# Kernel tuning notes

Measured on AMD Instinct MI355X. Metric: run time of the kernel, lower is better.

## Reference

```python
import jax, jax.numpy as jnp
import numpy as np


def setup_inputs() -> dict:
    key = jax.random.key(0)
    k1, k2 = jax.random.split(key)
    x = jax.random.normal(k1, (8, 128, 192, 192), dtype=jnp.float32)  # [n, c, h, w]
    K = jax.random.normal(k2, (8, 128, 128), dtype=jnp.float32)      # [n, Q, c]
    return {"x": x, "K": K}


def reference(x, K):
    n, c, h, w = x.shape
    xf = x.reshape(n, c, h * w)                      # [n, c, HW]
    # scores: [n, HW, Q] = x^T @ K^T (unscaled)
    y = jnp.einsum("ncs,nqc->nsq", xf, K)
    # softmax over spatial dim (HW), matching torch.softmax(y, dim=1)
    y = jax.nn.softmax(y, axis=1)
    # summary: [n, Q, c] = y^T @ x^T
    summary = jnp.einsum("nsq,ncs->nqc", y, xf)
    return summary
```

## Files before the change

### kernel.cpp

```cpp
#include <hip/hip_runtime.h>
#include <cstdint>


#define HW_DIM 36864
#define L2E 1.44269504088896340736f

typedef _Float16 half8 __attribute__((ext_vector_type(8)));
typedef float f32x16 __attribute__((ext_vector_type(16)));

#if __has_builtin(__builtin_amdgcn_exp2f)
#define EXP2(x) __builtin_amdgcn_exp2f(x)
#else
#define EXP2(x) exp2f(x)
#endif

#define BARRIER_LDS_ONLY() asm volatile("s_waitcnt lgkmcnt(0)\ns_barrier" ::: "memory")

__device__ __forceinline__ unsigned pk2(float a, float b) {
    auto h = __builtin_amdgcn_cvt_pkrtz(a, b);
    unsigned u; __builtin_memcpy(&u, &h, 4); return u;
}
__device__ __forceinline__ half8 mk8(unsigned a, unsigned b, unsigned c, unsigned d) {
    union { unsigned u[4]; half8 h; } t;
    t.u[0] = a; t.u[1] = b; t.u[2] = c; t.u[3] = d; return t.h;
}
__device__ __forceinline__ void pl32swap(unsigned &a, unsigned &b) {
    const bool lo = (threadIdx.x & 63) < 32;
    unsigned send = lo ? a : b;
    unsigned recv = (unsigned)__shfl_xor((int)send, 32);
    a = lo ? recv : a;
    b = lo ? b : recv;
}


__global__ __launch_bounds__(256, 3)
void flash_f16(const float* __restrict__ xg, const float* __restrict__ Kg,
               float* __restrict__ wsm, float* __restrict__ wsl,
               float* __restrict__ wacc, int SC, int sPerBlock)
{
    __shared__ __align__(16) char smem[16384];

    const int tid  = threadIdx.x;
    const int lane = tid & 63;
    const int qt   = tid >> 6;
    const int l31  = lane & 31;
    const int g    = lane >> 5;

    const int n  = blockIdx.y;
    const int sc = blockIdx.x;

    half8 kh[8];
    {
        const float* kp = Kg + ((size_t)n * 128 + 32 * qt + l31) * 128 + g * 8;
        #pragma unroll
        for (int ks = 0; ks < 8; ++ks) {
            float4 a = *(const float4*)(kp + ks * 16);
            float4 b = *(const float4*)(kp + ks * 16 + 4);
            float f[8] = {a.x, a.y, a.z, a.w, b.x, b.y, b.z, b.w};
            #pragma unroll
            for (int j = 0; j < 8; ++j) kh[ks][j] = (_Float16)(f[j] * L2E);
        }
    }

    const int c0   = (tid >> 3) << 2;
    const int sOff = (tid & 7) << 2;
    const float* xrow0 = xg + (size_t)n * 128 * HW_DIM + (size_t)c0 * HW_DIM
                         + (size_t)sc * sPerBlock + sOff;

    float4 stg[4];

    auto stage_write = [&]() {
        float fv[4][4] = {
            {stg[0].x, stg[0].y, stg[0].z, stg[0].w},
            {stg[1].x, stg[1].y, stg[1].z, stg[1].w},
            {stg[2].x, stg[2].y, stg[2].z, stg[2].w},
            {stg[3].x, stg[3].y, stg[3].z, stg[3].w}};
        #pragma unroll
        for (int r = 0; r < 4; ++r) {
            const int c = c0 + r;
            int off = 8192 + c * 64 + ((((sOff >> 3) ^ (c & 3))) << 4) + (sOff & 7) * 2;
            *(uint2*)(smem + off) = make_uint2(pk2(fv[r][0], fv[r][1]),
                                               pk2(fv[r][2], fv[r][3]));
        }
        #pragma unroll
        for (int j = 0; j < 4; ++j) {
            const int s = sOff + j;
            int off = s * 256 + ((((c0 >> 3) ^ (s & 15))) << 4) + (c0 & 7) * 2;
            *(uint2*)(smem + off) = make_uint2(pk2(fv[0][j], fv[1][j]),
                                               pk2(fv[2][j], fv[3][j]));
        }
    };

    f32x16 oacc[4];
    #pragma unroll
    for (int ct = 0; ct < 4; ++ct)
        #pragma unroll
        for (int r = 0; r < 16; ++r) oacc[ct][r] = 0.f;
    float m_run = -1e30f, l_run = 0.f;

    const int nT = sPerBlock >> 5;

    #pragma unroll
    for (int r = 0; r < 4; ++r) stg[r] = *(const float4*)(xrow0 + (size_t)r * HW_DIM);

    for (int t = 0; t < nT; ++t) {
        stage_write();
        if (t + 1 < nT) {
            const float* xr = xrow0 + (size_t)(t + 1) * 32;
            #pragma unroll
            for (int r = 0; r < 4; ++r) stg[r] = *(const float4*)(xr + (size_t)r * HW_DIM);
        }
        BARRIER_LDS_ONLY();

        f32x16 sa0, sa1;
        #pragma unroll
        for (int r = 0; r < 16; ++r) { sa0[r] = 0.f; sa1[r] = 0.f; }
        __builtin_amdgcn_s_setprio(1);
        #pragma unroll
        for (int ks = 0; ks < 8; ++ks) {
            int off = l31 * 256 + ((((ks << 1) | g) ^ (l31 & 15)) << 4);
            half8 xh = *(const half8*)(smem + off);
            if (ks & 1) sa1 = __builtin_amdgcn_mfma_f32_32x32x16_f16(xh, kh[ks], sa1, 0, 0, 0);
            else        sa0 = __builtin_amdgcn_mfma_f32_32x32x16_f16(xh, kh[ks], sa0, 0, 0, 0);
        }
        __builtin_amdgcn_s_setprio(0);
        float sv[16];
        #pragma unroll
        for (int r = 0; r < 16; ++r) sv[r] = sa0[r] + sa1[r];

        float m01 = fmaxf(sv[0], sv[1]),  m23 = fmaxf(sv[2], sv[3]);
        float m45 = fmaxf(sv[4], sv[5]),  m67 = fmaxf(sv[6], sv[7]);
        float m89 = fmaxf(sv[8], sv[9]),  mab = fmaxf(sv[10], sv[11]);
        float mcd = fmaxf(sv[12], sv[13]), mef = fmaxf(sv[14], sv[15]);
        float tm = fmaxf(fmaxf(fmaxf(m01, m23), fmaxf(m45, m67)),
                         fmaxf(fmaxf(m89, mab), fmaxf(mcd, mef)));
        tm = fmaxf(tm, __shfl_xor(tm, 32));
        if (__any(tm > m_run + 11.5f)) {
            float mnew = fmaxf(m_run, tm);
            float rr = EXP2(m_run - mnew);
            m_run = mnew;
            l_run *= rr;
            #pragma unroll
            for (int ct = 0; ct < 4; ++ct)
                #pragma unroll
                for (int r = 0; r < 16; ++r) oacc[ct][r] *= rr;
        }
        float pw[16];
        #pragma unroll
        for (int r = 0; r < 16; ++r) pw[r] = EXP2(sv[r] - m_run);
        float rs = ((pw[0] + pw[1]) + (pw[2] + pw[3])) + ((pw[4] + pw[5]) + (pw[6] + pw[7]));
        rs += ((pw[8] + pw[9]) + (pw[10] + pw[11])) + ((pw[12] + pw[13]) + (pw[14] + pw[15]));
        rs += __shfl_xor(rs, 32);
        l_run += rs;

        unsigned P00 = pk2(pw[0],  pw[1]),  P01 = pk2(pw[2],  pw[3]);
        unsigned P10 = pk2(pw[4],  pw[5]),  P11 = pk2(pw[6],  pw[7]);
        unsigned P20 = pk2(pw[8],  pw[9]),  P21 = pk2(pw[10], pw[11]);
        unsigned P30 = pk2(pw[12], pw[13]), P31 = pk2(pw[14], pw[15]);
        pl32swap(P10, P00);
        pl32swap(P11, P01);
        pl32swap(P30, P20);
        pl32swap(P31, P21);
        half8 bw0 = mk8(P00, P01, P10, P11);
        half8 bw1 = mk8(P20, P21, P30, P31);

        __builtin_amdgcn_s_setprio(1);
        #pragma unroll
        for (int kst = 0; kst < 2; ++kst) {
            half8 bw = kst ? bw1 : bw0;
            int blk = 2 * kst + g;
            #pragma unroll
            for (int ct = 0; ct < 4; ++ct) {
                int crow = 32 * ct + l31;
                half8 xa = *(const half8*)(smem + 8192 + crow * 64
                                           + ((blk ^ (crow & 3)) << 4));
                oacc[ct] = __builtin_amdgcn_mfma_f32_32x32x16_f16(xa, bw, oacc[ct], 0, 0, 0);
            }
        }
        __builtin_amdgcn_s_setprio(0);
        BARRIER_LDS_ONLY();
    }

    const size_t wb = ((size_t)(n * SC + sc)) * 16384;
    if (lane < 32) {
        wsm[(size_t)(n * SC + sc) * 128 + 32 * qt + lane] = m_run;
        wsl[(size_t)(n * SC + sc) * 128 + 32 * qt + lane] = l_run;
    }
    #pragma unroll
    for (int ct = 0; ct < 4; ++ct)
        #pragma unroll
        for (int r = 0; r < 16; ++r) {
            int c = 32 * ct + (r & 3) + 8 * (r >> 2) + 4 * g;
            wacc[wb + (size_t)c * 128 + 32 * qt + l31] = oacc[ct][r];
        }
}

__global__ __launch_bounds__(256)
void combine3(const float* __restrict__ wsm, const float* __restrict__ wsl,
              const float* __restrict__ wacc, float* __restrict__ out, int SC)
{
    const int n  = blockIdx.y;
    const int cb = blockIdx.x;
    const int t  = threadIdx.x;
    const int q  = t & 127;
    const int c  = cb * 2 + (t >> 7);

    const float* mp = wsm + (size_t)n * SC * 128 + q;
    const float* lp = wsl + (size_t)n * SC * 128 + q;
    const float* wp = wacc + ((size_t)n * SC * 128 + c) * 128 + q;

    float m0 = -1e30f, m1 = -1e30f, m2 = -1e30f, m3 = -1e30f;
    int s = 0;
    for (; s + 4 <= SC; s += 4) {
        m0 = fmaxf(m0, mp[(size_t)(s + 0) * 128]);
        m1 = fmaxf(m1, mp[(size_t)(s + 1) * 128]);
        m2 = fmaxf(m2, mp[(size_t)(s + 2) * 128]);
        m3 = fmaxf(m3, mp[(size_t)(s + 3) * 128]);
    }
    for (; s < SC; ++s) m0 = fmaxf(m0, mp[(size_t)s * 128]);
    const float mm = fmaxf(fmaxf(m0, m1), fmaxf(m2, m3));

    float L0 = 0.f, L1 = 0.f, a0 = 0.f, a1 = 0.f;
    s = 0;
    for (; s + 2 <= SC; s += 2) {
        float e0 = EXP2(mp[(size_t)(s + 0) * 128] - mm);
        float e1 = EXP2(mp[(size_t)(s + 1) * 128] - mm);
        L0 += e0 * lp[(size_t)(s + 0) * 128];
        L1 += e1 * lp[(size_t)(s + 1) * 128];
        a0 += e0 * wp[(size_t)(s + 0) * 16384];
        a1 += e1 * wp[(size_t)(s + 1) * 16384];
    }
    for (; s < SC; ++s) {
        float e = EXP2(mp[(size_t)s * 128] - mm);
        L0 += e * lp[(size_t)s * 128];
        a0 += e * wp[(size_t)s * 16384];
    }
    out[((size_t)n * 128 + q) * 128 + c] = (a0 + a1) / (L0 + L1);
}

extern "C" void kernel_launch(void* const* d_in, const int* in_sizes, int n_in,
                              void* d_out, int out_size, void* d_ws, size_t ws_size,
                              hipStream_t stream)
{
    (void)in_sizes; (void)n_in; (void)out_size;
    const float* x = (const float*)d_in[0];
    const float* K = (const float*)d_in[1];
    float* out = (float*)d_out;

    static const int scList[] = {96, 72, 64, 48, 36, 32, 24, 16, 12, 8, 6, 4, 2, 1};
    int SC = 1;
    for (int i = 0; i < 14; ++i) {
        size_t need = (size_t)8 * scList[i] * (16384 + 256) * sizeof(float);
        if (need <= ws_size) { SC = scList[i]; break; }
    }
    const int sPerBlock = HW_DIM / SC;

    float* wsm = (float*)d_ws;
    float* wsl = wsm + (size_t)8 * SC * 128;
    float* wa  = wsl + (size_t)8 * SC * 128;

    flash_f16<<<dim3(SC, 8), 256, 0, stream>>>(x, K, wsm, wsl, wa, SC, sPerBlock);
    combine3<<<dim3(64, 8), 256, 0, stream>>>(wsm, wsl, wa, out, SC);
}
```

Baseline: 70.08 us.

## Store partial accumulators as bf16, raise split count and occupancy, move prefetch

Partial per-split output accumulators are written to the workspace as bf16 instead of fp32, halving the traffic between the flash kernel and the combine kernel. This allows a larger split count (128), giving more blocks over the spatial dimension. Launch bounds are raised to 4 waves per SIMD, the two alternating score accumulators are merged into one, and the next-tile global prefetch moves after the score MFMAs. The bf16 rounding of partial sums loses precision, and register pressure may cause spills.

```diff
diff --git a/kernel.cpp b/kernel.cpp
--- a/kernel.cpp
+++ b/kernel.cpp
@@ -23,6 +23,13 @@
 __device__ __forceinline__ half8 mk8(unsigned a, unsigned b, unsigned c, unsigned d) {
     union { unsigned u[4]; half8 h; } t;
     t.u[0] = a; t.u[1] = b; t.u[2] = c; t.u[3] = d; return t.h;
+}
+__device__ __forceinline__ unsigned short bf16r(float f) {
+    unsigned u = __float_as_uint(f);
+    return (unsigned short)((u + 0x7FFFu + ((u >> 16) & 1u)) >> 16);
+}
+__device__ __forceinline__ float bf16f(unsigned short b) {
+    return __uint_as_float(((unsigned)b) << 16);
 }
 __device__ __forceinline__ void pl32swap(unsigned &a, unsigned &b) {
     const bool lo = (threadIdx.x & 63) < 32;
@@ -33,10 +40,10 @@
 }
 
 
-__global__ __launch_bounds__(256, 3)
+__global__ __launch_bounds__(256, 4)
 void flash_f16(const float* __restrict__ xg, const float* __restrict__ Kg,
                float* __restrict__ wsm, float* __restrict__ wsl,
-               float* __restrict__ wacc, int SC, int sPerBlock)
+               unsigned short* __restrict__ wacc, int SC, int sPerBlock)
 {
     __shared__ __align__(16) char smem[16384];
 
@@ -105,28 +112,29 @@
 
     for (int t = 0; t < nT; ++t) {
         stage_write();
-        if (t + 1 < nT) {
-            const float* xr = xrow0 + (size_t)(t + 1) * 32;
-            #pragma unroll
-            for (int r = 0; r < 4; ++r) stg[r] = *(const float4*)(xr + (size_t)r * HW_DIM);
-        }
         BARRIER_LDS_ONLY();
 
-        f32x16 sa0, sa1;
-        #pragma unroll
-        for (int r = 0; r < 16; ++r) { sa0[r] = 0.f; sa1[r] = 0.f; }
+        f32x16 sa;
+        #pragma unroll
+        for (int r = 0; r < 16; ++r) sa[r] = 0.f;
         __builtin_amdgcn_s_setprio(1);
         #pragma unroll
         for (int ks = 0; ks < 8; ++ks) {
             int off = l31 * 256 + ((((ks << 1) | g) ^ (l31 & 15)) << 4);
             half8 xh = *(const half8*)(smem + off);
-            if (ks & 1) sa1 = __builtin_amdgcn_mfma_f32_32x32x16_f16(xh, kh[ks], sa1, 0, 0, 0);
-            else        sa0 = __builtin_amdgcn_mfma_f32_32x32x16_f16(xh, kh[ks], sa0, 0, 0, 0);
+            sa = __builtin_amdgcn_mfma_f32_32x32x16_f16(xh, kh[ks], sa, 0, 0, 0);
         }
         __builtin_amdgcn_s_setprio(0);
+
+        if (t + 1 < nT) {
+            const float* xr = xrow0 + (size_t)(t + 1) * 32;
+            #pragma unroll
+            for (int r = 0; r < 4; ++r) stg[r] = *(const float4*)(xr + (size_t)r * HW_DIM);
+        }
+
         float sv[16];
         #pragma unroll
-        for (int r = 0; r < 16; ++r) sv[r] = sa0[r] + sa1[r];
+        for (int r = 0; r < 16; ++r) sv[r] = sa[r];
 
         float m01 = fmaxf(sv[0], sv[1]),  m23 = fmaxf(sv[2], sv[3]);
         float m45 = fmaxf(sv[4], sv[5]),  m67 = fmaxf(sv[6], sv[7]);
@@ -191,13 +199,13 @@
         #pragma unroll
         for (int r = 0; r < 16; ++r) {
             int c = 32 * ct + (r & 3) + 8 * (r >> 2) + 4 * g;
-            wacc[wb + (size_t)c * 128 + 32 * qt + l31] = oacc[ct][r];
+            wacc[wb + (size_t)c * 128 + 32 * qt + l31] = bf16r(oacc[ct][r]);
         }
 }
 
 __global__ __launch_bounds__(256)
 void combine3(const float* __restrict__ wsm, const float* __restrict__ wsl,
-              const float* __restrict__ wacc, float* __restrict__ out, int SC)
+              const unsigned short* __restrict__ wacc, float* __restrict__ out, int SC)
 {
     const int n  = blockIdx.y;
     const int cb = blockIdx.x;
@@ -207,7 +215,7 @@
 
     const float* mp = wsm + (size_t)n * SC * 128 + q;
     const float* lp = wsl + (size_t)n * SC * 128 + q;
-    const float* wp = wacc + ((size_t)n * SC * 128 + c) * 128 + q;
+    const unsigned short* wp = wacc + ((size_t)n * SC * 16384) + (size_t)c * 128 + q;
 
     float m0 = -1e30f, m1 = -1e30f, m2 = -1e30f, m3 = -1e30f;
     int s = 0;
@@ -227,13 +235,13 @@
         float e1 = EXP2(mp[(size_t)(s + 1) * 128] - mm);
         L0 += e0 * lp[(size_t)(s + 0) * 128];
         L1 += e1 * lp[(size_t)(s + 1) * 128];
-        a0 += e0 * wp[(size_t)(s + 0) * 16384];
-        a1 += e1 * wp[(size_t)(s + 1) * 16384];
+        a0 += e0 * bf16f(wp[(size_t)(s + 0) * 16384]);
+        a1 += e1 * bf16f(wp[(size_t)(s + 1) * 16384]);
     }
     for (; s < SC; ++s) {
         float e = EXP2(mp[(size_t)s * 128] - mm);
         L0 += e * lp[(size_t)s * 128];
-        a0 += e * wp[(size_t)s * 16384];
+        a0 += e * bf16f(wp[(size_t)s * 16384]);
     }
     out[((size_t)n * 128 + q) * 128 + c] = (a0 + a1) / (L0 + L1);
 }
@@ -247,17 +255,17 @@
     const float* K = (const float*)d_in[1];
     float* out = (float*)d_out;
 
-    static const int scList[] = {96, 72, 64, 48, 36, 32, 24, 16, 12, 8, 6, 4, 2, 1};
+    static const int scList[] = {128, 96, 72, 64, 48, 36, 32, 24, 16, 12, 8, 6, 4, 2, 1};
     int SC = 1;
-    for (int i = 0; i < 14; ++i) {
-        size_t need = (size_t)8 * scList[i] * (16384 + 256) * sizeof(float);
+    for (int i = 0; i < 15; ++i) {
+        size_t need = (size_t)scList[i] * 270336;
         if (need <= ws_size) { SC = scList[i]; break; }
     }
     const int sPerBlock = HW_DIM / SC;
 
     float* wsm = (float*)d_ws;
     float* wsl = wsm + (size_t)8 * SC * 128;
-    float* wa  = wsl + (size_t)8 * SC * 128;
+    unsigned short* wa = (unsigned short*)(wsl + (size_t)8 * SC * 128);
 
     flash_f16<<<dim3(SC, 8), 256, 0, stream>>>(x, K, wsm, wsl, wa, SC, sPerBlock);
     combine3<<<dim3(64, 8), 256, 0, stream>>>(wsm, wsl, wa, out, SC);
```

Result: slower. 113.6 us (+62.0%).
